# Kernel optimization log

Measured on AMD Instinct MI355X. Metric: run time of the kernel, lower is better.

Reference implementation:

```python
import jax, jax.numpy as jnp
import numpy as np

N, NFEAT, NHID, NCLASS, H1 = 4096, 512, 64, 16, 8
GAIN = 1.414  # xavier gain used by the torch module
NEG_SLOPE = 0.2
MASK_VAL = -1e10


def _xavier(k, shape):
    fan_in, fan_out = shape[-2], shape[-1]
    lim = GAIN * (6.0 / (fan_in + fan_out)) ** 0.5
    return jax.random.uniform(k, shape, jnp.float32, -lim, lim)


def setup_inputs() -> dict:
    key = jax.random.key(0)
    ks = jax.random.split(key, 10)
    return {
        "x": jax.random.normal(ks[0], (N, NFEAT), jnp.float32),
        "adj": jax.random.randint(ks[1], (N, N), 0, 2, jnp.int32),
        # layer-1 parameters, stacked over H1 heads
        "W1": _xavier(ks[2], (H1, NFEAT, NHID)),
        "b1": jnp.zeros((H1, NHID), jnp.float32),
        "as1": _xavier(ks[3], (H1, NHID, 1))[..., 0],
        "an1": _xavier(ks[4], (H1, NHID, 1))[..., 0],
        # layer-2 parameters (single head, input = H1*NHID due to concat)
        "W2": _xavier(ks[5], (H1 * NHID, NCLASS)),
        "b2": jnp.zeros((NCLASS,), jnp.float32),
        "as2": _xavier(ks[6], (NCLASS, 1))[:, 0],
        "an2": _xavier(ks[7], (NCLASS, 1))[:, 0],
    }


def gat_layer(X, adj_pos, W, b, a_s, a_n):
    # X: [N, Fin], W: [Fin, Fout], a_s/a_n: [Fout], adj_pos: [N, N] bool
    feats = X @ W                                        # [N, Fout]
    s = feats @ a_s                                      # [N]
    nb = feats @ a_n                                     # [N]
    attn = jax.nn.leaky_relu(s[:, None] + nb[None, :], NEG_SLOPE)  # [N, N]
    attn = jnp.where(adj_pos, attn, MASK_VAL)
    attn = jax.nn.softmax(attn, axis=-1)
    # dropout on attn/feats is a no-op in eval mode
    return attn @ feats + b                              # [N, Fout]


def reference(x, adj, W1, b1, as1, an1, W2, b2, as2, an2):
    adj_pos = adj > 0
    # x dropout is a no-op in eval mode
    layer1 = jax.vmap(gat_layer, in_axes=(None, None, 0, 0, 0, 0))
    h = jax.nn.relu(layer1(x, adj_pos, W1, b1, as1, an1))    # [H1, N, NHID]
    h = jnp.transpose(h, (1, 0, 2)).reshape(N, H1 * NHID)    # concat heads on dim 1
    h = jax.nn.elu(h)
    out = jax.nn.relu(gat_layer(h, adj_pos, W2, b2, as2, an2))  # [N, NCLASS]
    return jax.nn.log_softmax(out, axis=1)
```

## Files before the change

kernel.cpp:

```cpp
#include <hip/hip_runtime.h>

#define NN 4096
#define NFEAT 512
#define NHID 64
#define H1 8
#define NCLS 16
#define BND 40.0f
#define VSTR 72
#define FSCL 4096.0f

typedef short bf16x8 __attribute__((ext_vector_type(8)));
typedef _Float16 f16x8 __attribute__((ext_vector_type(8)));
typedef _Float16 h2 __attribute__((ext_vector_type(2)));
typedef __fp16 fp16v2 __attribute__((ext_vector_type(2)));
typedef float f32x4 __attribute__((ext_vector_type(4)));

__device__ __forceinline__ unsigned short f2bf(float f) {
    unsigned u = __float_as_uint(f);
    u += 0x7fffu + ((u >> 16) & 1u);
    return (unsigned short)(u >> 16);
}
__device__ __forceinline__ float leaky(float v) { return fmaxf(v, 0.2f * v); }
__device__ __forceinline__ unsigned pkbf(float lo, float hi) {
    return __builtin_amdgcn_perm(__float_as_uint(hi) + 0x8000u,
                                 __float_as_uint(lo) + 0x8000u, 0x07060302u);
}
__device__ __forceinline__ unsigned pkh(float lo, float hi) {
    union { fp16v2 h; unsigned u; } c;
    c.h = __builtin_amdgcn_cvt_pkrtz(lo, hi);
    return c.u;
}
__device__ __forceinline__ h2 uash(unsigned u) { union { unsigned u; h2 h; } c; c.u = u; return c.h; }
__device__ __forceinline__ unsigned hasu(h2 h) { union { unsigned u; h2 h; } c; c.h = h; return c.u; }
__device__ __forceinline__ bf16x8 mk8(unsigned a, unsigned b, unsigned c, unsigned d) {
    union { unsigned u[4]; bf16x8 v; } cv;
    cv.u[0] = a; cv.u[1] = b; cv.u[2] = c; cv.u[3] = d; return cv.v;
}
__device__ __forceinline__ f16x8 mk8h(unsigned a, unsigned b, unsigned c, unsigned d) {
    union { unsigned u[4]; f16x8 v; } cv;
    cv.u[0] = a; cv.u[1] = b; cv.u[2] = c; cv.u[3] = d; return cv.v;
}
__device__ __forceinline__ unsigned fkey(float f) {
    const unsigned u = __float_as_uint(f);
    return (u >> 31) ? ~u : (u | 0x80000000u);
}
__device__ __forceinline__ float funkey(unsigned k) {
    return __uint_as_float((k & 0x80000000u) ? (k ^ 0x80000000u) : ~k);
}

__global__ __launch_bounds__(256)
void k_prep(const int* __restrict__ adj, unsigned long long* __restrict__ bits,
            const float* __restrict__ W1, unsigned short* __restrict__ w1f,
            const float* __restrict__ x, unsigned short* __restrict__ xh,
            unsigned* __restrict__ nbkey)
{
    __shared__ float wt[64][65];
    const int t = threadIdx.x, bx = blockIdx.x;
    if (bx < 2 * NN) {
        const int row = bx >> 1, half = bx & 1;
        const int j0 = half * 2048 + t * 8;
        const int* ap = adj + (size_t)row * NN + j0;
        const int4 v0 = *(const int4*)(ap);
        const int4 v1 = *(const int4*)(ap + 4);
        const unsigned b = (unsigned)(v0.x > 0)        | ((unsigned)(v0.y > 0) << 1)
                         | ((unsigned)(v0.z > 0) << 2) | ((unsigned)(v0.w > 0) << 3)
                         | ((unsigned)(v1.x > 0) << 4) | ((unsigned)(v1.y > 0) << 5)
                         | ((unsigned)(v1.z > 0) << 6) | ((unsigned)(v1.w > 0) << 7);
        ((unsigned char*)bits)[(size_t)row * 512 + (j0 >> 3)] = (unsigned char)b;
        return;
    }
    if (bx == 2 * NN + 64 + 512) {
        if (t < H1) nbkey[t] = 0u;
        return;
    }
    if (bx >= 2 * NN + 64) {
        const int b = bx - (2 * NN + 64);
        #pragma unroll
        for (int i = 0; i < 4; ++i) {
            const int f4 = b * 1024 + i * 256 + t;
            const float4 v = ((const float4*)x)[f4];
            uint2 w; w.x = pkh(v.x, v.y); w.y = pkh(v.z, v.w);
            ((uint2*)xh)[f4] = w;
        }
        return;
    }
    const int idx = bx - 2 * NN;
    const int kt = idx & 7, h = idx >> 3;
    #pragma unroll
    for (int i = 0; i < 4; ++i) {
        const int f = t + 256 * i;
        const int r = f >> 4, c4 = f & 15;
        const float4 v = *(const float4*)(W1 + ((size_t)(h * NFEAT) + kt * 64 + r) * NHID + c4 * 4);
        wt[r][c4 * 4 + 0] = v.x; wt[r][c4 * 4 + 1] = v.y;
        wt[r][c4 * 4 + 2] = v.z; wt[r][c4 * 4 + 3] = v.w;
    }
    __syncthreads();
    #pragma unroll
    for (int s = 0; s < 2; ++s) {
        const int o = t + s * 256;
        const int kg2 = o >> 8, rem = o & 255;
        const int nt = rem >> 6, lane2 = rem & 63;
        const int qq = lane2 >> 4, nn = lane2 & 15;
        const int kl = kg2 * 32 + qq * 8;
        const int c = nt * 16 + nn;
        uint4 w;
        w.x = pkh(wt[kl + 0][c], wt[kl + 1][c]);
        w.y = pkh(wt[kl + 2][c], wt[kl + 3][c]);
        w.z = pkh(wt[kl + 4][c], wt[kl + 5][c]);
        w.w = pkh(wt[kl + 6][c], wt[kl + 7][c]);
        *(uint4*)(w1f + (((size_t)h * 16 + kt * 2 + kg2) * 4 + nt) * 512 + lane2 * 8) = w;
    }
}

__global__ __launch_bounds__(256)
void k_feats1(const unsigned short* __restrict__ xh, const unsigned short* __restrict__ w1f,
              const float* __restrict__ as1, const float* __restrict__ an1,
              unsigned short* __restrict__ f1bT, float* __restrict__ s1,
              float* __restrict__ nb1, unsigned* __restrict__ nbkey)
{
    const int t = threadIdx.x, wv = t >> 6, lane = t & 63;
    const int q = lane >> 4, n = lane & 15;
    const int h = blockIdx.x, R0 = blockIdx.y * 64;
    const int row = R0 + wv * 16 + n;
    const unsigned short* ap = xh + (size_t)row * NFEAT;
    const unsigned short* wp = w1f + (size_t)h * 16 * 4 * 512 + lane * 8;
    f32x4 acc[4] = {{0.f,0.f,0.f,0.f},{0.f,0.f,0.f,0.f},{0.f,0.f,0.f,0.f},{0.f,0.f,0.f,0.f}};
    #pragma unroll 4
    for (int kg = 0; kg < 16; ++kg) {
        const f16x8 af = *(const f16x8*)(ap + kg * 32 + q * 8);
        #pragma unroll
        for (int nt = 0; nt < 4; ++nt) {
            const f16x8 bf = *(const f16x8*)(wp + (size_t)(kg * 4 + nt) * 512);
            acc[nt] = __builtin_amdgcn_mfma_f32_16x16x32_f16(af, bf, acc[nt], 0, 0, 0);
        }
    }
    #pragma unroll
    for (int nt = 0; nt < 4; ++nt) {
        uint2 w;
        w.x = pkh(acc[nt][0], acc[nt][1]);
        w.y = pkh(acc[nt][2], acc[nt][3]);
        *(uint2*)(f1bT + ((size_t)h * NHID + nt * 16 + n) * NN + R0 + wv * 16 + q * 4) = w;
    }
    float asv[4], anv[4];
    #pragma unroll
    for (int nt = 0; nt < 4; ++nt) {
        asv[nt] = as1[h * NHID + nt * 16 + n];
        anv[nt] = an1[h * NHID + nt * 16 + n];
    }
    float pmax = -1e30f;
    #pragma unroll
    for (int i = 0; i < 4; ++i) {
        float ps = acc[0][i]*asv[0] + acc[1][i]*asv[1] + acc[2][i]*asv[2] + acc[3][i]*asv[3];
        float pn = acc[0][i]*anv[0] + acc[1][i]*anv[1] + acc[2][i]*anv[2] + acc[3][i]*anv[3];
        #pragma unroll
        for (int off = 8; off > 0; off >>= 1) {
            ps += __shfl_xor(ps, off, 64);
            pn += __shfl_xor(pn, off, 64);
        }
        pmax = fmaxf(pmax, pn);
        if (n == 0) {
            const int idx = R0 + wv * 16 + q * 4 + i;
            s1[h * NN + idx] = ps;
            nb1[h * NN + idx] = pn;
        }
    }
    pmax = fmaxf(pmax, __shfl_xor(pmax, 16, 64));
    pmax = fmaxf(pmax, __shfl_xor(pmax, 32, 64));
    if (lane == 0) atomicMax(nbkey + h, fkey(pmax));
}

__global__ __launch_bounds__(256)
void k_fact1(const float* __restrict__ nb1, const unsigned* __restrict__ nbkey,
             unsigned short* __restrict__ F12)
{
    const int h = blockIdx.x, ck = blockIdx.y, t = threadIdx.x;
    const float mx = funkey(nbkey[h]);
    const int j = ck * 512 + t * 2;
    const float d0 = nb1[h * NN + j] - mx, d1 = nb1[h * NN + j + 1] - mx;
    unsigned short* base = F12 + ((size_t)h * 512 + (j >> 3)) * 16 + (j & 7);
    *(unsigned*)(base)     = pkh(FSCL * __expf(d0),        FSCL * __expf(d1));
    *(unsigned*)(base + 8) = pkh(FSCL * __expf(0.2f * d0), FSCL * __expf(0.2f * d1));
}

__global__ __launch_bounds__(512, 4)
void k_gat1(const unsigned short* __restrict__ f1bT, const float* __restrict__ s1,
            const unsigned short* __restrict__ F12, const unsigned long long* __restrict__ abits,
            const float* __restrict__ b1, const unsigned* __restrict__ nbkey,
            unsigned short* __restrict__ hcatb)
{
    __shared__ __align__(16) char smem[4 * 2 * 64 * VSTR * 2];
    unsigned short* vT = (unsigned short*)smem;

    const int t = threadIdx.x, wv = t >> 6, lane = t & 63;
    const int q = lane >> 4, n = lane & 15;
    const int rg = wv >> 2, jq = wv & 3;
    const int h = blockIdx.x, R0 = blockIdx.y * 64;
    const int rowA = R0 + rg * 32 + n;
    const int rowB = rowA + 16;
    const float mh = funkey(nbkey[h]);
    const float vA = s1[h * NN + rowA] + mh, mhA = leaky(vA);
    const float vB = s1[h * NN + rowB] + mh, mhB = leaky(vB);
    const float E1Af = __expf(vA - mhA), E2Af = __expf(0.2f * vA - mhA);
    const float E1Bf = __expf(vB - mhB), E2Bf = __expf(0.2f * vB - mhB);
    const h2 E1A = {(_Float16)E1Af, (_Float16)E1Af};
    const h2 E2A = {(_Float16)E2Af, (_Float16)E2Af};
    const h2 E1B = {(_Float16)E1Bf, (_Float16)E1Bf};
    const h2 E2B = {(_Float16)E2Bf, (_Float16)E2Bf};
    const unsigned long long* arowA = abits + (size_t)rowA * 64;
    const unsigned long long* arowB = abits + (size_t)rowB * 64;
    const unsigned short* Fp = F12 + (size_t)h * 512 * 16;

    const int stile = t >> 7;
    const int sc0 = (t & 127) >> 3, sj8 = t & 7;
    const unsigned short* sbase = f1bT + (size_t)h * NHID * NN + (size_t)sc0 * NN + sj8 * 8;
    const int dof = sc0 * VSTR + sj8 * 8;

    f32x4 accA[4] = {{0.f,0.f,0.f,0.f},{0.f,0.f,0.f,0.f},{0.f,0.f,0.f,0.f},{0.f,0.f,0.f,0.f}};
    f32x4 accB[4] = {{0.f,0.f,0.f,0.f},{0.f,0.f,0.f,0.f},{0.f,0.f,0.f,0.f},{0.f,0.f,0.f,0.f}};
    float lsA = 0.f, lsB = 0.f;

    {
        const int js = stile * 1024;
        int4 v0 = *(const int4*)(sbase + js);
        int4 v1 = *(const int4*)(sbase + (size_t)16 * NN + js);
        int4 v2 = *(const int4*)(sbase + (size_t)32 * NN + js);
        int4 v3 = *(const int4*)(sbase + (size_t)48 * NN + js);
        unsigned short* d = vT + (stile * 2 + 0) * (64 * VSTR) + dof;
        *(int4*)(d) = v0;
        *(int4*)(d + 16 * VSTR) = v1;
        *(int4*)(d + 32 * VSTR) = v2;
        *(int4*)(d + 48 * VSTR) = v3;
    }
    __syncthreads();

    for (int it = 0; it < 16; ++it) {
        const int db = it & 1;
        int4 p0, p1, p2, p3;
        if (it < 15) {
            const int js = stile * 1024 + (it + 1) * 64;
            p0 = *(const int4*)(sbase + js);
            p1 = *(const int4*)(sbase + (size_t)16 * NN + js);
            p2 = *(const int4*)(sbase + (size_t)32 * NN + js);
            p3 = *(const int4*)(sbase + (size_t)48 * NN + js);
        }
        const int j0 = jq * 1024 + it * 64;
        const unsigned long long aA = arowA[j0 >> 6];
        const unsigned long long aB = arowB[j0 >> 6];
        const unsigned short* tbase = vT + (jq * 2 + db) * (64 * VSTR);
        #pragma unroll
        for (int ch = 0; ch < 2; ++ch) {
            const int kb = ch * 32 + q * 8;
            const unsigned short* fg = Fp + (size_t)((j0 + kb) >> 3) * 16;
            const uint4 f1w = *(const uint4*)(fg);
            const uint4 f2w = *(const uint4*)(fg + 8);
            const unsigned bA = (unsigned)(aA >> kb) & 0xffu;
            const unsigned bB = (unsigned)(aB >> kb) & 0xffu;
            unsigned uA[4], uB[4];
            h2 sA2 = {(_Float16)0, (_Float16)0};
            h2 sB2 = {(_Float16)0, (_Float16)0};
            #pragma unroll
            for (int jp = 0; jp < 4; ++jp) {
                const h2 f1 = uash(((const unsigned*)&f1w)[jp]);
                const h2 f2 = uash(((const unsigned*)&f2w)[jp]);
                const unsigned mA = ((bA >> (2*jp)) & 1u) * 0x3C00u
                                  + ((bA >> (2*jp+1)) & 1u) * 0x3C000000u;
                const unsigned mB = ((bB >> (2*jp)) & 1u) * 0x3C00u
                                  + ((bB >> (2*jp+1)) & 1u) * 0x3C000000u;
                h2 pA = __builtin_elementwise_max(E1A * f1, E2A * f2) * uash(mA);
                h2 pB = __builtin_elementwise_max(E1B * f1, E2B * f2) * uash(mB);
                sA2 += pA; sB2 += pB;
                uA[jp] = hasu(pA); uB[jp] = hasu(pB);
            }
            lsA += (float)sA2[0] + (float)sA2[1];
            lsB += (float)sB2[0] + (float)sB2[1];
            const f16x8 afA = mk8h(uA[0], uA[1], uA[2], uA[3]);
            const f16x8 afB = mk8h(uB[0], uB[1], uB[2], uB[3]);
            #pragma unroll
            for (int nt = 0; nt < 4; ++nt) {
                const f16x8 bf = *(const f16x8*)(tbase + (nt * 16 + n) * VSTR + kb);
                accA[nt] = __builtin_amdgcn_mfma_f32_16x16x32_f16(afA, bf, accA[nt], 0, 0, 0);
                accB[nt] = __builtin_amdgcn_mfma_f32_16x16x32_f16(afB, bf, accB[nt], 0, 0, 0);
            }
        }
        if (it < 15) {
            unsigned short* d = vT + (stile * 2 + (db ^ 1)) * (64 * VSTR) + dof;
            *(int4*)(d) = p0;
            *(int4*)(d + 16 * VSTR) = p1;
            *(int4*)(d + 32 * VSTR) = p2;
            *(int4*)(d + 48 * VSTR) = p3;
        }
        __syncthreads();
    }

    lsA += __shfl_xor(lsA, 16, 64); lsA += __shfl_xor(lsA, 32, 64);
    lsB += __shfl_xor(lsB, 16, 64); lsB += __shfl_xor(lsB, 32, 64);

    float* cmbf = (float*)smem;
    float* lwf  = (float*)(smem + 69632);
    #pragma unroll
    for (int nt = 0; nt < 4; ++nt)
        #pragma unroll
        for (int i = 0; i < 4; ++i) {
            cmbf[((size_t)jq * 64 + rg * 32 + q * 4 + i) * 68 + nt * 16 + n] = accA[nt][i];
            cmbf[((size_t)jq * 64 + rg * 32 + 16 + q * 4 + i) * 68 + nt * 16 + n] = accB[nt][i];
        }
    if (q == 0) {
        lwf[jq * 64 + rg * 32 + n] = lsA;
        lwf[jq * 64 + rg * 32 + 16 + n] = lsB;
    }
    __syncthreads();

    const int col = t & 63, r8 = t >> 6;
    const float bv = b1[h * NHID + col];
    #pragma unroll
    for (int rr = 0; rr < 8; ++rr) {
        const int r = r8 * 8 + rr;
        float tot = 0.f, lt = 0.f;
        #pragma unroll
        for (int jj = 0; jj < 4; ++jj) {
            tot += cmbf[((size_t)jj * 64 + r) * 68 + col];
            lt  += lwf[jj * 64 + r];
        }
        hcatb[(size_t)(R0 + r) * (H1 * NHID) + h * NHID + col] =
            f2bf(fmaxf(tot / lt + bv, 0.f));
    }
}

__global__ __launch_bounds__(128)
void k_feats2(const unsigned short* __restrict__ hcatb, const float* __restrict__ W2,
              const float* __restrict__ as2, const float* __restrict__ an2,
              unsigned short* __restrict__ f2bT, float* __restrict__ s2,
              float* __restrict__ F1b, float* __restrict__ F2b)
{
    __shared__ __align__(16) unsigned short w2T[NCLS][520];
    const int t = threadIdx.x, wv = t >> 6, lane = t & 63;
    const int q = lane >> 4, n = lane & 15;
    #pragma unroll
    for (int i = 0; i < 16; ++i) {
        const int f4 = t + 128 * i;
        const float4 v = ((const float4*)W2)[f4];
        const int k = f4 >> 2, c0 = (f4 & 3) * 4;
        w2T[c0 + 0][k] = f2bf(v.x); w2T[c0 + 1][k] = f2bf(v.y);
        w2T[c0 + 2][k] = f2bf(v.z); w2T[c0 + 3][k] = f2bf(v.w);
    }
    __syncthreads();

    const int R0 = blockIdx.x * 32;
    const int row = R0 + wv * 16 + n;
    const unsigned short* ap = hcatb + (size_t)row * NFEAT;
    f32x4 acc = {0.f, 0.f, 0.f, 0.f};
    #pragma unroll 4
    for (int k0 = 0; k0 < NFEAT; k0 += 32) {
        const bf16x8 af = *(const bf16x8*)(ap + k0 + q * 8);
        const bf16x8 bf = *(const bf16x8*)&w2T[n][k0 + q * 8];
        acc = __builtin_amdgcn_mfma_f32_16x16x32_bf16(af, bf, acc, 0, 0, 0);
    }
    uint2 w;
    w.x = pkbf(acc[0], acc[1]);
    w.y = pkbf(acc[2], acc[3]);
    *(uint2*)(f2bT + (size_t)n * NN + R0 + wv * 16 + q * 4) = w;
    const float asv = as2[n], anv = an2[n];
    #pragma unroll
    for (int i = 0; i < 4; ++i) {
        float ps = acc[i] * asv, pn = acc[i] * anv;
        #pragma unroll
        for (int off = 8; off > 0; off >>= 1) {
            ps += __shfl_xor(ps, off, 64);
            pn += __shfl_xor(pn, off, 64);
        }
        if (n == 0) {
            const int idx = R0 + wv * 16 + q * 4 + i;
            s2[idx] = ps;
            F1b[idx] = __expf(pn - BND);
            F2b[idx] = __expf(0.2f * (pn - BND));
        }
    }
}

__global__ __launch_bounds__(1024)
void k_gat2(const unsigned short* __restrict__ f2bT, const float* __restrict__ s2,
            const float* __restrict__ F1, const float* __restrict__ F2,
            const unsigned long long* __restrict__ abits, const float* __restrict__ b2,
            float* __restrict__ out)
{
    __shared__ float cmb[16][16][17];
    __shared__ float lw[16][16];
    const int t = threadIdx.x, wv = t >> 6, lane = t & 63;
    const int q = lane >> 4, n = lane & 15;
    const int R0 = blockIdx.x * 16, row = R0 + n;
    const float v = s2[row] + BND, mhat = leaky(v);
    const float E1 = __expf(v - mhat), E2 = __expf(0.2f * v - mhat);
    const unsigned long long* arow = abits + (size_t)row * 64;

    f32x4 acc = {0.f, 0.f, 0.f, 0.f};
    float lsum = 0.f;
    const int jbeg = wv * 256;
    for (int j0 = jbeg; j0 < jbeg + 256; j0 += 64) {
        const unsigned long long a64 = arow[j0 >> 6];
        #pragma unroll
        for (int ch = 0; ch < 2; ++ch) {
            const int kb = ch * 32 + q * 8;
            const float4 f1a = *(const float4*)(F1 + j0 + kb);
            const float4 f1b = *(const float4*)(F1 + j0 + kb + 4);
            const float4 f2a = *(const float4*)(F2 + j0 + kb);
            const float4 f2b = *(const float4*)(F2 + j0 + kb + 4);
            const float F1v[8] = {f1a.x, f1a.y, f1a.z, f1a.w, f1b.x, f1b.y, f1b.z, f1b.w};
            const float F2v[8] = {f2a.x, f2a.y, f2a.z, f2a.w, f2b.x, f2b.y, f2b.z, f2b.w};
            const unsigned b8 = (unsigned)(a64 >> kb) & 0xffu;
            unsigned au[4];
            #pragma unroll
            for (int jp = 0; jp < 4; ++jp) {
                float p0 = fmaxf(E1 * F1v[2*jp],   E2 * F2v[2*jp]);
                float p1 = fmaxf(E1 * F1v[2*jp+1], E2 * F2v[2*jp+1]);
                p0 = ((b8 >> (2*jp)) & 1u) ? p0 : 0.f;
                p1 = ((b8 >> (2*jp+1)) & 1u) ? p1 : 0.f;
                lsum += p0 + p1;
                au[jp] = pkbf(p0, p1);
            }
            const bf16x8 af = mk8(au[0], au[1], au[2], au[3]);
            const bf16x8 bf = *(const bf16x8*)(f2bT + (size_t)n * NN + j0 + kb);
            acc = __builtin_amdgcn_mfma_f32_16x16x32_bf16(af, bf, acc, 0, 0, 0);
        }
    }
    lsum += __shfl_xor(lsum, 16, 64);
    lsum += __shfl_xor(lsum, 32, 64);
    #pragma unroll
    for (int i = 0; i < 4; ++i) cmb[wv][q * 4 + i][n] = acc[i];
    if (q == 0) lw[wv][n] = lsum;
    __syncthreads();

    if (t < 256) {
        const int r = t >> 4, c = t & 15;
        float tot = 0.f, lt = 0.f;
        #pragma unroll
        for (int w16 = 0; w16 < 16; ++w16) { tot += cmb[w16][r][c]; lt += lw[w16][r]; }
        float val = fmaxf(tot / lt + b2[c], 0.f);
        float mx = val;
        #pragma unroll
        for (int off = 1; off < 16; off <<= 1) mx = fmaxf(mx, __shfl_xor(mx, off, 64));
        const float e = __expf(val - mx);
        float se = e;
        #pragma unroll
        for (int off = 1; off < 16; off <<= 1) se += __shfl_xor(se, off, 64);
        out[(size_t)(R0 + r) * NCLS + c] = val - mx - __logf(se);
    }
}

extern "C" void kernel_launch(void* const* d_in, const int* in_sizes, int n_in,
                              void* d_out, int out_size, void* d_ws, size_t ws_size,
                              hipStream_t stream)
{
    const float* x   = (const float*)d_in[0];
    const int*   adj = (const int*)  d_in[1];
    const float* W1  = (const float*)d_in[2];
    const float* b1  = (const float*)d_in[3];
    const float* as1 = (const float*)d_in[4];
    const float* an1 = (const float*)d_in[5];
    const float* W2  = (const float*)d_in[6];
    const float* b2  = (const float*)d_in[7];
    const float* as2 = (const float*)d_in[8];
    const float* an2 = (const float*)d_in[9];
    float* out = (float*)d_out;

    char* ws = (char*)d_ws;
    unsigned long long* abits = (unsigned long long*)(ws);
    unsigned short* f1bT  = (unsigned short*)(ws + (2u << 20));
    unsigned short* xh    = (unsigned short*)(ws + (6u << 20));
    unsigned short* hcatb = xh;
    unsigned short* w1f   = (unsigned short*)(ws + (10u << 20));
    char* ws2 = ws + (10u << 20) + (512u << 10);
    float* s1   = (float*)(ws2);
    float* nb1  = (float*)(ws2 + (128u << 10));
    unsigned short* F12 = (unsigned short*)(ws2 + (256u << 10));
    unsigned short* f2bT = (unsigned short*)(ws2 + (384u << 10));
    float* s2   = (float*)(ws2 + (512u << 10));
    float* F1b  = (float*)(ws2 + (528u << 10));
    float* F2b  = (float*)(ws2 + (544u << 10));
    unsigned* nbkey = (unsigned*)(ws2 + (560u << 10));

    k_prep  <<<dim3(2 * NN + 64 + 512 + 1), 256, 0, stream>>>(adj, abits, W1, w1f, x, xh, nbkey);
    k_feats1<<<dim3(H1, NN / 64),  256, 0, stream>>>(xh, w1f, as1, an1, f1bT, s1, nb1, nbkey);
    k_fact1 <<<dim3(H1, 8),        256, 0, stream>>>(nb1, nbkey, F12);
    k_gat1  <<<dim3(H1, NN / 64),  512, 0, stream>>>(f1bT, s1, F12, abits, b1, nbkey, hcatb);
    k_feats2<<<dim3(NN / 32),      128, 0, stream>>>(hcatb, W2, as2, an2, f2bT, s2, F1b, F2b);
    k_gat2  <<<dim3(NN / 16),      1024, 0, stream>>>(f2bT, s2, F1b, F2b, abits, b2, out);
}
```

Before: 220.1 us.

## Give each wave a private swizzled LDS tile in gat1 and ballot-pack adjacency

```diff
diff --git a/kernel.cpp b/kernel.cpp
--- a/kernel.cpp
+++ b/kernel.cpp
@@ -6,7 +6,6 @@
 #define H1 8
 #define NCLS 16
 #define BND 40.0f
-#define VSTR 72
 #define FSCL 4096.0f
 
 typedef short bf16x8 __attribute__((ext_vector_type(8)));
@@ -56,25 +55,21 @@
 {
     __shared__ float wt[64][65];
     const int t = threadIdx.x, bx = blockIdx.x;
-    if (bx < 2 * NN) {
-        const int row = bx >> 1, half = bx & 1;
-        const int j0 = half * 2048 + t * 8;
-        const int* ap = adj + (size_t)row * NN + j0;
-        const int4 v0 = *(const int4*)(ap);
-        const int4 v1 = *(const int4*)(ap + 4);
-        const unsigned b = (unsigned)(v0.x > 0)        | ((unsigned)(v0.y > 0) << 1)
-                         | ((unsigned)(v0.z > 0) << 2) | ((unsigned)(v0.w > 0) << 3)
-                         | ((unsigned)(v1.x > 0) << 4) | ((unsigned)(v1.y > 0) << 5)
-                         | ((unsigned)(v1.z > 0) << 6) | ((unsigned)(v1.w > 0) << 7);
-        ((unsigned char*)bits)[(size_t)row * 512 + (j0 >> 3)] = (unsigned char)b;
+    if (bx < NN) {
+        const int wv = t >> 6, lane = t & 63;
+        const int* ap = adj + (size_t)bx * NN;
+        for (int w = wv; w < 64; w += 4) {
+            unsigned long long m = __ballot(ap[w * 64 + lane] > 0);
+            if (lane == 0) bits[(size_t)bx * 64 + w] = m;
+        }
         return;
     }
-    if (bx == 2 * NN + 64 + 512) {
+    if (bx == NN + 64 + 512) {
         if (t < H1) nbkey[t] = 0u;
         return;
     }
-    if (bx >= 2 * NN + 64) {
-        const int b = bx - (2 * NN + 64);
+    if (bx >= NN + 64) {
+        const int b = bx - (NN + 64);
         #pragma unroll
         for (int i = 0; i < 4; ++i) {
             const int f4 = b * 1024 + i * 256 + t;
@@ -84,7 +79,7 @@
         }
         return;
     }
-    const int idx = bx - 2 * NN;
+    const int idx = bx - NN;
     const int kt = idx & 7, h = idx >> 3;
     #pragma unroll
     for (int i = 0; i < 4; ++i) {
@@ -182,21 +177,19 @@
     *(unsigned*)(base + 8) = pkh(FSCL * __expf(0.2f * d0), FSCL * __expf(0.2f * d1));
 }
 
-__global__ __launch_bounds__(512, 4)
+__global__ __launch_bounds__(256, 4)
 void k_gat1(const unsigned short* __restrict__ f1bT, const float* __restrict__ s1,
             const unsigned short* __restrict__ F12, const unsigned long long* __restrict__ abits,
             const float* __restrict__ b1, const unsigned* __restrict__ nbkey,
             unsigned short* __restrict__ hcatb)
 {
-    __shared__ __align__(16) char smem[4 * 2 * 64 * VSTR * 2];
+    __shared__ __align__(16) char smem[4 * 4096 * 2];
     unsigned short* vT = (unsigned short*)smem;
 
-    const int t = threadIdx.x, wv = t >> 6, lane = t & 63;
+    const int t = threadIdx.x, jq = t >> 6, lane = t & 63;
     const int q = lane >> 4, n = lane & 15;
-    const int rg = wv >> 2, jq = wv & 3;
-    const int h = blockIdx.x, R0 = blockIdx.y * 64;
-    const int rowA = R0 + rg * 32 + n;
-    const int rowB = rowA + 16;
+    const int h = blockIdx.x, R0 = blockIdx.y * 32;
+    const int rowA = R0 + n, rowB = rowA + 16;
     const float mh = funkey(nbkey[h]);
     const float vA = s1[h * NN + rowA] + mh, mhA = leaky(vA);
     const float vB = s1[h * NN + rowB] + mh, mhB = leaky(vB);
@@ -210,43 +203,33 @@
     const unsigned long long* arowB = abits + (size_t)rowB * 64;
     const unsigned short* Fp = F12 + (size_t)h * 512 * 16;
 
-    const int stile = t >> 7;
-    const int sc0 = (t & 127) >> 3, sj8 = t & 7;
-    const unsigned short* sbase = f1bT + (size_t)h * NHID * NN + (size_t)sc0 * NN + sj8 * 8;
-    const int dof = sc0 * VSTR + sj8 * 8;
+    const int sc0 = lane >> 3, sj8 = lane & 7;
+    const int swz = sj8 ^ sc0;
+    const unsigned short* sbase = f1bT + (size_t)h * NHID * NN + (size_t)sc0 * NN
+                                + (size_t)jq * 1024 + sj8 * 8;
+    unsigned short* myT = vT + jq * 4096;
 
     f32x4 accA[4] = {{0.f,0.f,0.f,0.f},{0.f,0.f,0.f,0.f},{0.f,0.f,0.f,0.f},{0.f,0.f,0.f,0.f}};
     f32x4 accB[4] = {{0.f,0.f,0.f,0.f},{0.f,0.f,0.f,0.f},{0.f,0.f,0.f,0.f},{0.f,0.f,0.f,0.f}};
     float lsA = 0.f, lsB = 0.f;
 
-    {
-        const int js = stile * 1024;
-        int4 v0 = *(const int4*)(sbase + js);
-        int4 v1 = *(const int4*)(sbase + (size_t)16 * NN + js);
-        int4 v2 = *(const int4*)(sbase + (size_t)32 * NN + js);
-        int4 v3 = *(const int4*)(sbase + (size_t)48 * NN + js);
-        unsigned short* d = vT + (stile * 2 + 0) * (64 * VSTR) + dof;
-        *(int4*)(d) = v0;
-        *(int4*)(d + 16 * VSTR) = v1;
-        *(int4*)(d + 32 * VSTR) = v2;
-        *(int4*)(d + 48 * VSTR) = v3;
-    }
-    __syncthreads();
+    int4 pr[8];
+    #pragma unroll
+    for (int m = 0; m < 8; ++m) pr[m] = *(const int4*)(sbase + (size_t)(8 * m) * NN);
 
     for (int it = 0; it < 16; ++it) {
-        const int db = it & 1;
-        int4 p0, p1, p2, p3;
+        #pragma unroll
+        for (int m = 0; m < 8; ++m)
+            *(int4*)(myT + (sc0 + 8 * m) * 64 + swz * 8) = pr[m];
         if (it < 15) {
-            const int js = stile * 1024 + (it + 1) * 64;
-            p0 = *(const int4*)(sbase + js);
-            p1 = *(const int4*)(sbase + (size_t)16 * NN + js);
-            p2 = *(const int4*)(sbase + (size_t)32 * NN + js);
-            p3 = *(const int4*)(sbase + (size_t)48 * NN + js);
+            const int js = (it + 1) * 64;
+            #pragma unroll
+            for (int m = 0; m < 8; ++m)
+                pr[m] = *(const int4*)(sbase + (size_t)(8 * m) * NN + js);
         }
         const int j0 = jq * 1024 + it * 64;
         const unsigned long long aA = arowA[j0 >> 6];
         const unsigned long long aB = arowB[j0 >> 6];
-        const unsigned short* tbase = vT + (jq * 2 + db) * (64 * VSTR);
         #pragma unroll
         for (int ch = 0; ch < 2; ++ch) {
             const int kb = ch * 32 + q * 8;
@@ -277,52 +260,48 @@
             const f16x8 afB = mk8h(uB[0], uB[1], uB[2], uB[3]);
             #pragma unroll
             for (int nt = 0; nt < 4; ++nt) {
-                const f16x8 bf = *(const f16x8*)(tbase + (nt * 16 + n) * VSTR + kb);
+                const int c = nt * 16 + n;
+                const f16x8 bf = *(const f16x8*)(myT + c * 64 + (((ch * 4 + q) ^ (n & 7)) << 3));
                 accA[nt] = __builtin_amdgcn_mfma_f32_16x16x32_f16(afA, bf, accA[nt], 0, 0, 0);
                 accB[nt] = __builtin_amdgcn_mfma_f32_16x16x32_f16(afB, bf, accB[nt], 0, 0, 0);
             }
         }
-        if (it < 15) {
-            unsigned short* d = vT + (stile * 2 + (db ^ 1)) * (64 * VSTR) + dof;
-            *(int4*)(d) = p0;
-            *(int4*)(d + 16 * VSTR) = p1;
-            *(int4*)(d + 32 * VSTR) = p2;
-            *(int4*)(d + 48 * VSTR) = p3;
-        }
-        __syncthreads();
     }
 
     lsA += __shfl_xor(lsA, 16, 64); lsA += __shfl_xor(lsA, 32, 64);
     lsB += __shfl_xor(lsB, 16, 64); lsB += __shfl_xor(lsB, 32, 64);
 
-    float* cmbf = (float*)smem;
-    float* lwf  = (float*)(smem + 69632);
+    __syncthreads();
+    _Float16* cmbh = (_Float16*)smem;
+    float* lwf = (float*)(smem + 17408);
     #pragma unroll
     for (int nt = 0; nt < 4; ++nt)
         #pragma unroll
         for (int i = 0; i < 4; ++i) {
-            cmbf[((size_t)jq * 64 + rg * 32 + q * 4 + i) * 68 + nt * 16 + n] = accA[nt][i];
-            cmbf[((size_t)jq * 64 + rg * 32 + 16 + q * 4 + i) * 68 + nt * 16 + n] = accB[nt][i];
+            cmbh[((size_t)jq * 32 + q * 4 + i) * 68 + nt * 16 + n] =
+                (_Float16)(accA[nt][i] * 0x1p-12f);
+            cmbh[((size_t)jq * 32 + 16 + q * 4 + i) * 68 + nt * 16 + n] =
+                (_Float16)(accB[nt][i] * 0x1p-12f);
         }
     if (q == 0) {
-        lwf[jq * 64 + rg * 32 + n] = lsA;
-        lwf[jq * 64 + rg * 32 + 16 + n] = lsB;
+        lwf[jq * 32 + n] = lsA;
+        lwf[jq * 32 + 16 + n] = lsB;
     }
     __syncthreads();
 
-    const int col = t & 63, r8 = t >> 6;
+    const int col = t & 63, rbase = (t >> 6) * 8;
     const float bv = b1[h * NHID + col];
     #pragma unroll
     for (int rr = 0; rr < 8; ++rr) {
-        const int r = r8 * 8 + rr;
+        const int r = rbase + rr;
         float tot = 0.f, lt = 0.f;
         #pragma unroll
         for (int jj = 0; jj < 4; ++jj) {
-            tot += cmbf[((size_t)jj * 64 + r) * 68 + col];
-            lt  += lwf[jj * 64 + r];
+            tot += (float)cmbh[((size_t)jj * 32 + r) * 68 + col];
+            lt  += lwf[jj * 32 + r];
         }
         hcatb[(size_t)(R0 + r) * (H1 * NHID) + h * NHID + col] =
-            f2bf(fmaxf(tot / lt + bv, 0.f));
+            f2bf(fmaxf(tot * 4096.f / lt + bv, 0.f));
     }
 }
 
@@ -478,10 +457,10 @@
     float* F2b  = (float*)(ws2 + (544u << 10));
     unsigned* nbkey = (unsigned*)(ws2 + (560u << 10));
 
-    k_prep  <<<dim3(2 * NN + 64 + 512 + 1), 256, 0, stream>>>(adj, abits, W1, w1f, x, xh, nbkey);
+    k_prep  <<<dim3(NN + 64 + 512 + 1), 256, 0, stream>>>(adj, abits, W1, w1f, x, xh, nbkey);
     k_feats1<<<dim3(H1, NN / 64),  256, 0, stream>>>(xh, w1f, as1, an1, f1bT, s1, nb1, nbkey);
     k_fact1 <<<dim3(H1, 8),        256, 0, stream>>>(nb1, nbkey, F12);
-    k_gat1  <<<dim3(H1, NN / 64),  512, 0, stream>>>(f1bT, s1, F12, abits, b1, nbkey, hcatb);
+    k_gat1  <<<dim3(H1, NN / 32),  256, 0, stream>>>(f1bT, s1, F12, abits, b1, nbkey, hcatb);
     k_feats2<<<dim3(NN / 32),      128, 0, stream>>>(hcatb, W2, as2, an2, f2bT, s2, F1b, F2b);
     k_gat2  <<<dim3(NN / 16),      1024, 0, stream>>>(f2bT, s2, F1b, F2b, abits, b2, out);
 }
```

After: 382.9 us. 74.0% more time.
